# Kernel tuning notes

Hardware: AMD Instinct MI355X
Metric: run time of the kernel (lower is better)

## Reference

```python
import jax, jax.numpy as jnp
import numpy as np

INV_SQRT2 = np.float32(2.0 ** -0.5)
EPS = 1e-5


def _bn5(x, g, b, m, v):
    # inference-mode BatchNorm3d over channel axis 1 of NCDHW
    r = (1, -1, 1, 1, 1)
    return (x - m.reshape(r)) * (g.reshape(r) * jax.lax.rsqrt(v.reshape(r) + EPS)) + b.reshape(r)


def _conv3d(x, w, b, dil=1, pad=0):
    out = jax.lax.conv_general_dilated(
        x, w, window_strides=(1, 1, 1), padding=[(pad, pad)] * 3,
        rhs_dilation=(dil, dil, dil),
        dimension_numbers=('NCDHW', 'OIDHW', 'NCDHW'))
    return out + b.reshape(1, -1, 1, 1, 1)


def _haar_dwt2(x):
    # pywt dwt2(x, 'haar', axes=(-3,-2)) for even-length axes.
    # axis -3 (D): a = approx, d = detail (pywt sign: (x0 - x1)/sqrt2)
    a = (x[:, :, 0::2] + x[:, :, 1::2]) * INV_SQRT2
    d = (x[:, :, 0::2] - x[:, :, 1::2]) * INV_SQRT2
    # axis -2 (H)
    LL = (a[:, :, :, 0::2] + a[:, :, :, 1::2]) * INV_SQRT2  # 'aa'
    HL = (a[:, :, :, 0::2] - a[:, :, :, 1::2]) * INV_SQRT2  # 'ad'
    LH = (d[:, :, :, 0::2] + d[:, :, :, 1::2]) * INV_SQRT2  # 'da'
    HH = (d[:, :, :, 0::2] - d[:, :, :, 1::2]) * INV_SQRT2  # 'dd'
    return LL, LH, HL, HH


def setup_inputs() -> dict:
    key = jax.random.key(0)
    ks = jax.random.split(key, 12)
    B, C1, D, H, W = 2, 60, 128, 128, 64
    CH, R = 64, 4  # gate channels, CH // reduction_ratio
    f32 = jnp.float32
    inp = {
        'x1': jax.random.normal(ks[0], (B, C1, D // 2, H // 2, W), f32),
        'x2': jax.random.normal(ks[1], (B, 1, D, H, W), f32),
        # BatchNorm3d(4) on dwt features
        'bn_g': jnp.ones(4, f32), 'bn_b': jnp.zeros(4, f32),
        'bn_m': jnp.zeros(4, f32), 'bn_v': jnp.ones(4, f32),
        # BAM channel gate: Linear(64->4), BN1d(4), Linear(4->64)
        'cg_w1': jax.random.normal(ks[2], (R, CH), f32) * 0.05,
        'cg_b1': jnp.zeros(R, f32),
        'cg_bng': jnp.ones(R, f32), 'cg_bnb': jnp.zeros(R, f32),
        'cg_bnm': jnp.zeros(R, f32), 'cg_bnv': jnp.ones(R, f32),
        'cg_w2': jax.random.normal(ks[3], (CH, R), f32) * 0.05,
        'cg_b2': jnp.zeros(CH, f32),
        # BAM spatial gate
        'sg_w0': jax.random.normal(ks[4], (R, CH, 1, 1, 1), f32) * 0.05,
        'sg_b0': jnp.zeros(R, f32),
        'sg_g0': jnp.ones(R, f32), 'sg_be0': jnp.zeros(R, f32),
        'sg_m0': jnp.zeros(R, f32), 'sg_v0': jnp.ones(R, f32),
        'sg_w1': jax.random.normal(ks[5], (R, R, 3, 3, 3), f32) * 0.05,
        'sg_b1': jnp.zeros(R, f32),
        'sg_g1': jnp.ones(R, f32), 'sg_be1': jnp.zeros(R, f32),
        'sg_m1': jnp.zeros(R, f32), 'sg_v1': jnp.ones(R, f32),
        'sg_w2': jax.random.normal(ks[6], (R, R, 3, 3, 3), f32) * 0.05,
        'sg_b2': jnp.zeros(R, f32),
        'sg_g2': jnp.ones(R, f32), 'sg_be2': jnp.zeros(R, f32),
        'sg_m2': jnp.zeros(R, f32), 'sg_v2': jnp.ones(R, f32),
        'sg_w3': jax.random.normal(ks[7], (1, R, 1, 1, 1), f32) * 0.05,
        'sg_b3': jnp.zeros(1, f32),
    }
    return inp


def reference(x1, x2, bn_g, bn_b, bn_m, bn_v,
              cg_w1, cg_b1, cg_bng, cg_bnb, cg_bnm, cg_bnv, cg_w2, cg_b2,
              sg_w0, sg_b0, sg_g0, sg_be0, sg_m0, sg_v0,
              sg_w1, sg_b1, sg_g1, sg_be1, sg_m1, sg_v1,
              sg_w2, sg_b2, sg_g2, sg_be2, sg_m2, sg_v2,
              sg_w3, sg_b3):
    LL, LH, HL, HH = _haar_dwt2(x2)
    dwt = jnp.concatenate([LL, LH, HL, HH], axis=1)          # [B,4,D/2,H/2,W]
    dwt = jax.nn.relu(_bn5(dwt, bn_g, bn_b, bn_m, bn_v))
    feat = jnp.concatenate([dwt, x1], axis=1)                # [B,64,D/2,H/2,W]

    # BAM channel gate
    pooled = feat.mean(axis=(2, 3, 4))                        # [B,64]
    h = pooled @ cg_w1.T + cg_b1
    h = jax.nn.relu((h - cg_bnm) * (cg_bng * jax.lax.rsqrt(cg_bnv + EPS)) + cg_bnb)
    att_c = (h @ cg_w2.T + cg_b2)[:, :, None, None, None]     # [B,64,1,1,1]

    # BAM spatial gate
    s = jax.nn.relu(_bn5(_conv3d(feat, sg_w0, sg_b0), sg_g0, sg_be0, sg_m0, sg_v0))
    s = jax.nn.relu(_bn5(_conv3d(s, sg_w1, sg_b1, dil=4, pad=4), sg_g1, sg_be1, sg_m1, sg_v1))
    s = jax.nn.relu(_bn5(_conv3d(s, sg_w2, sg_b2, dil=4, pad=4), sg_g2, sg_be2, sg_m2, sg_v2))
    att_s = _conv3d(s, sg_w3, sg_b3)                          # [B,1,D/2,H/2,W]

    scale = 1.0 + jax.nn.sigmoid(att_c + att_s)
    return (feat * scale, LL)
```

## Files before the change

kernel.cpp:

```cpp
#include <hip/hip_runtime.h>
#include <math.h>

#define EPSBN 1e-5f

typedef float f32x2 __attribute__((ext_vector_type(2)));
typedef float f32x4 __attribute__((ext_vector_type(4)));

constexpr int B   = 2;
constexpr int C1  = 60;
constexpr int NV  = 64 * 64 * 64;
constexpr int NBa = NV / 1024;
constexpr int NBc = NV / 512;

__global__ __launch_bounds__(256) void kA(
    const float* __restrict__ x1, const float* __restrict__ x2,
    const float* __restrict__ bn_g, const float* __restrict__ bn_b,
    const float* __restrict__ bn_m, const float* __restrict__ bn_v,
    const float* __restrict__ sg_w0, const float* __restrict__ sg_b0,
    const float* __restrict__ sg_g0, const float* __restrict__ sg_be0,
    const float* __restrict__ sg_m0, const float* __restrict__ sg_v0,
    float* __restrict__ s0,
    float* __restrict__ part)
{
    __shared__ float wsumq[64][65];

    const int tid = threadIdx.x;
    const int qid = tid >> 2;

    float dsc[4], dsh[4], c0A[4], c0B[4];
    #pragma unroll
    for (int r = 0; r < 4; ++r) {
        float d = bn_g[r] * rsqrtf(bn_v[r] + EPSBN);
        dsc[r] = d; dsh[r] = bn_b[r] - bn_m[r] * d;
        float sc = sg_g0[r] * rsqrtf(sg_v0[r] + EPSBN);
        c0A[r] = sc; c0B[r] = (sg_b0[r] - sg_m0[r]) * sc + sg_be0[r];
    }

    const int b = blockIdx.y;
    const int v = blockIdx.x * 1024 + tid * 4;
    const int x = v & 63, y = (v >> 6) & 63, z = v >> 12;

    const float* px2 = x2 + (size_t)b * (128 * 128 * 64);
    const size_t i00 = ((size_t)(2 * z) * 128 + 2 * y) * 64 + x;
    const float4 p00 = *(const float4*)(px2 + i00);
    const float4 p01 = *(const float4*)(px2 + i00 + 64);
    const float4 p10 = *(const float4*)(px2 + i00 + 8192);
    const float4 p11 = *(const float4*)(px2 + i00 + 8256);
    const float* q00 = (const float*)&p00; const float* q01 = (const float*)&p01;
    const float* q10 = (const float*)&p10; const float* q11 = (const float*)&p11;

    float tv[4][4];
    #pragma unroll
    for (int vi = 0; vi < 4; ++vi) {
        float a = q00[vi], bb = q01[vi], c = q10[vi], d = q11[vi];
        float LL = 0.5f * (a + bb + c + d);
        float LH = 0.5f * (a + bb - c - d);
        float HL = 0.5f * (a - bb + c - d);
        float HH = 0.5f * (a - bb - c + d);
        tv[vi][0] = fmaxf(LL * dsc[0] + dsh[0], 0.f);
        tv[vi][1] = fmaxf(LH * dsc[1] + dsh[1], 0.f);
        tv[vi][2] = fmaxf(HL * dsc[2] + dsh[2], 0.f);
        tv[vi][3] = fmaxf(HH * dsc[3] + dsh[3], 0.f);
    }

    float acc[4][4] = {};
    #pragma unroll
    for (int c = 0; c < 4; ++c) {
        #pragma unroll
        for (int vi = 0; vi < 4; ++vi) {
            float t = tv[vi][c];
            #pragma unroll
            for (int r = 0; r < 4; ++r) acc[vi][r] += sg_w0[r * 64 + c] * t;
        }
        float rs = tv[0][c] + tv[1][c] + tv[2][c] + tv[3][c];
        rs += __shfl_xor(rs, 1);
        rs += __shfl_xor(rs, 2);
        if ((tid & 3) == 0) wsumq[c][qid] = rs;
    }

    const float* px1 = x1 + (size_t)b * C1 * NV + v;
    #pragma unroll 4
    for (int c = 0; c < C1; ++c) {
        const float4 f = *(const float4*)(px1 + (size_t)c * NV);
        const float* fv = (const float*)&f;
        #pragma unroll
        for (int r = 0; r < 4; ++r) {
            const float w = sg_w0[r * 64 + 4 + c];
            #pragma unroll
            for (int vi = 0; vi < 4; ++vi) acc[vi][r] += w * fv[vi];
        }
        float rs = f.x + f.y + f.z + f.w;
        rs += __shfl_xor(rs, 1);
        rs += __shfl_xor(rs, 2);
        if ((tid & 3) == 0) wsumq[4 + c][qid] = rs;
    }

    float4* ps0 = (float4*)s0 + (size_t)b * NV + v;
    #pragma unroll
    for (int vi = 0; vi < 4; ++vi)
        ps0[vi] = make_float4(fmaxf(acc[vi][0] * c0A[0] + c0B[0], 0.f),
                              fmaxf(acc[vi][1] * c0A[1] + c0B[1], 0.f),
                              fmaxf(acc[vi][2] * c0A[2] + c0B[2], 0.f),
                              fmaxf(acc[vi][3] * c0A[3] + c0B[3], 0.f));

    __syncthreads();
    if (tid < 64) {
        const float* rowp = &wsumq[tid][0];
        float p = 0.f;
        #pragma unroll
        for (int i = 0; i < 64; ++i) p += rowp[i];
        part[((size_t)b * 64 + tid) * NBa + blockIdx.x] = p;
    }
}

__global__ __launch_bounds__(256) void kConv1(
    const float* __restrict__ sin_,
    const float* __restrict__ w, const float* __restrict__ bias,
    const float* __restrict__ g, const float* __restrict__ be,
    const float* __restrict__ m, const float* __restrict__ vv,
    const float* __restrict__ part,
    const float* __restrict__ cg_w1, const float* __restrict__ cg_b1,
    const float* __restrict__ cg_bng, const float* __restrict__ cg_bnb,
    const float* __restrict__ cg_bnm, const float* __restrict__ cg_bnv,
    const float* __restrict__ cg_w2, const float* __restrict__ cg_b2,
    float* __restrict__ ec,
    float* __restrict__ outp)
{
    const int tid = threadIdx.x;
    const int b = blockIdx.y;

    if (blockIdx.x == NBc) {
        __shared__ float pooled[64];
        __shared__ float h[4];
        const int c = tid >> 2, q = tid & 3;
        const float4* pp = (const float4*)(part + ((size_t)b * 64 + c) * NBa + q * 64);
        float sm = 0.f;
        #pragma unroll
        for (int i = 0; i < 16; ++i) { float4 f = pp[i]; sm += f.x + f.y + f.z + f.w; }
        sm += __shfl_xor(sm, 1);
        sm += __shfl_xor(sm, 2);
        if (q == 0) pooled[c] = sm * (1.0f / NV);
        __syncthreads();
        if (tid < 4) {
            float a = cg_b1[tid];
            for (int cc = 0; cc < 64; ++cc) a += pooled[cc] * cg_w1[tid * 64 + cc];
            float sc = cg_bng[tid] * rsqrtf(cg_bnv[tid] + EPSBN);
            h[tid] = fmaxf((a - cg_bnm[tid]) * sc + cg_bnb[tid], 0.f);
        }
        __syncthreads();
        if (tid < 64) {
            float a = cg_b2[tid];
            #pragma unroll
            for (int r = 0; r < 4; ++r) a += h[r] * cg_w2[tid * 4 + r];
            ec[b * 64 + tid] = __expf(-a);
        }
        return;
    }

    __shared__ float4 wl4[108];
    if (tid < 108) {
        const int t = tid >> 2, r = tid & 3;
        wl4[tid] = make_float4(w[r * 108 +      t], w[r * 108 +  27 + t],
                               w[r * 108 + 54 + t], w[r * 108 +  81 + t]);
    }
    float cAr[4], cBr[4];
    #pragma unroll
    for (int r = 0; r < 4; ++r) {
        float sc = g[r] * rsqrtf(vv[r] + EPSBN);
        cAr[r] = sc;
        cBr[r] = (bias[r] - m[r]) * sc + be[r];
    }
    __syncthreads();

    const int v = blockIdx.x * 512 + tid * 2;
    const int x = v & 63, y = (v >> 6) & 63, z = v >> 12;
    const float4* pin = (const float4*)sin_ + (size_t)b * NV;

    float acc[2][4] = {};
    #pragma unroll
    for (int kz = -1; kz <= 1; ++kz) {
        const int zz = z + 4 * kz;
        if ((unsigned)zz >= 64u) continue;
        #pragma unroll
        for (int ky = -1; ky <= 1; ++ky) {
            const int yy = y + 4 * ky;
            if ((unsigned)yy >= 64u) continue;
            #pragma unroll
            for (int kx = -1; kx <= 1; ++kx) {
                const int xx = x + 4 * kx;
                if ((unsigned)xx >= 64u) continue;
                const int t = (kz + 1) * 9 + (ky + 1) * 3 + (kx + 1);
                const int vt = zz * 4096 + yy * 64 + xx;
                const float4 w0 = wl4[t * 4 + 0];
                const float4 w1 = wl4[t * 4 + 1];
                const float4 w2 = wl4[t * 4 + 2];
                const float4 w3 = wl4[t * 4 + 3];
                #pragma unroll
                for (int vi = 0; vi < 2; ++vi) {
                    const float4 tap = pin[vt + vi];
                    acc[vi][0] += w0.x * tap.x + w0.y * tap.y + w0.z * tap.z + w0.w * tap.w;
                    acc[vi][1] += w1.x * tap.x + w1.y * tap.y + w1.z * tap.z + w1.w * tap.w;
                    acc[vi][2] += w2.x * tap.x + w2.y * tap.y + w2.z * tap.z + w2.w * tap.w;
                    acc[vi][3] += w3.x * tap.x + w3.y * tap.y + w3.z * tap.z + w3.w * tap.w;
                }
            }
        }
    }

    float4* po = (float4*)outp + (size_t)b * NV + v;
    #pragma unroll
    for (int vi = 0; vi < 2; ++vi)
        po[vi] = make_float4(fmaxf(acc[vi][0] * cAr[0] + cBr[0], 0.f),
                             fmaxf(acc[vi][1] * cAr[1] + cBr[1], 0.f),
                             fmaxf(acc[vi][2] * cAr[2] + cBr[2], 0.f),
                             fmaxf(acc[vi][3] * cAr[3] + cBr[3], 0.f));
}

__global__ __launch_bounds__(256) void kMulF(
    const float* __restrict__ x1,
    const float* __restrict__ x2,
    const float* __restrict__ bn_g, const float* __restrict__ bn_b,
    const float* __restrict__ bn_m, const float* __restrict__ bn_v,
    const float* __restrict__ s1,
    const float* __restrict__ w, const float* __restrict__ bias,
    const float* __restrict__ g, const float* __restrict__ be,
    const float* __restrict__ m, const float* __restrict__ vv,
    const float* __restrict__ w3, const float* __restrict__ b3,
    const float* __restrict__ ec,
    float* __restrict__ out0,
    float* __restrict__ outLL)
{
    const int tid = threadIdx.x;
    const int b = blockIdx.x >> 9;
    const int vb = (blockIdx.x & 511) * 512;

    __shared__ float4 wl4[108];
    __shared__ float ecs[64];
    __shared__ float esb[512];
    __shared__ float dwtb[512][4];
    if (tid < 108) {
        const int t = tid >> 2, r = tid & 3;
        wl4[tid] = make_float4(w[r * 108 +      t], w[r * 108 +  27 + t],
                               w[r * 108 + 54 + t], w[r * 108 +  81 + t]);
    }
    if (tid < 64) ecs[tid] = ec[b * 64 + tid];
    float cAr[4], cBr[4], w3l[4], dsc[4], dsh[4];
    #pragma unroll
    for (int r = 0; r < 4; ++r) {
        float sc = g[r] * rsqrtf(vv[r] + EPSBN);
        cAr[r] = sc;
        cBr[r] = (bias[r] - m[r]) * sc + be[r];
        w3l[r] = w3[r];
        float d = bn_g[r] * rsqrtf(bn_v[r] + EPSBN);
        dsc[r] = d; dsh[r] = bn_b[r] - bn_m[r] * d;
    }
    const float b3l = b3[0];
    __syncthreads();

    {
        const int v = vb + tid * 2;
        const int x = v & 63, y = (v >> 6) & 63, z = v >> 12;

        const float* px2 = x2 + (size_t)b * (128 * 128 * 64);
        const size_t i00 = ((size_t)(2 * z) * 128 + 2 * y) * 64 + x;
        const float2 p00 = *(const float2*)(px2 + i00);
        const float2 p01 = *(const float2*)(px2 + i00 + 64);
        const float2 p10 = *(const float2*)(px2 + i00 + 8192);
        const float2 p11 = *(const float2*)(px2 + i00 + 8256);
        const float* q00 = (const float*)&p00; const float* q01 = (const float*)&p01;
        const float* q10 = (const float*)&p10; const float* q11 = (const float*)&p11;
        float llv[2];
        #pragma unroll
        for (int vi = 0; vi < 2; ++vi) {
            float a = q00[vi], bb = q01[vi], c = q10[vi], d = q11[vi];
            float LL = 0.5f * (a + bb + c + d);
            float LH = 0.5f * (a + bb - c - d);
            float HL = 0.5f * (a - bb + c - d);
            float HH = 0.5f * (a - bb - c + d);
            llv[vi] = LL;
            float4 tv = make_float4(fmaxf(LL * dsc[0] + dsh[0], 0.f),
                                    fmaxf(LH * dsc[1] + dsh[1], 0.f),
                                    fmaxf(HL * dsc[2] + dsh[2], 0.f),
                                    fmaxf(HH * dsc[3] + dsh[3], 0.f));
            *(float4*)&dwtb[tid * 2 + vi][0] = tv;
        }
        {
            f32x2 ll2 = { llv[0], llv[1] };
            __builtin_nontemporal_store(ll2, (f32x2*)(outLL + (size_t)b * NV + v));
        }

        const float4* pin = (const float4*)s1 + (size_t)b * NV;
        float acc[2][4] = {};
        #pragma unroll
        for (int kz = -1; kz <= 1; ++kz) {
            const int zz = z + 4 * kz;
            if ((unsigned)zz >= 64u) continue;
            #pragma unroll
            for (int ky = -1; ky <= 1; ++ky) {
                const int yy = y + 4 * ky;
                if ((unsigned)yy >= 64u) continue;
                #pragma unroll
                for (int kx = -1; kx <= 1; ++kx) {
                    const int xx = x + 4 * kx;
                    if ((unsigned)xx >= 64u) continue;
                    const int t = (kz + 1) * 9 + (ky + 1) * 3 + (kx + 1);
                    const int vt = zz * 4096 + yy * 64 + xx;
                    const float4 w0 = wl4[t * 4 + 0];
                    const float4 w1 = wl4[t * 4 + 1];
                    const float4 w2 = wl4[t * 4 + 2];
                    const float4 w3q = wl4[t * 4 + 3];
                    #pragma unroll
                    for (int vi = 0; vi < 2; ++vi) {
                        const float4 tap = pin[vt + vi];
                        acc[vi][0] += w0.x * tap.x + w0.y * tap.y + w0.z * tap.z + w0.w * tap.w;
                        acc[vi][1] += w1.x * tap.x + w1.y * tap.y + w1.z * tap.z + w1.w * tap.w;
                        acc[vi][2] += w2.x * tap.x + w2.y * tap.y + w2.z * tap.z + w2.w * tap.w;
                        acc[vi][3] += w3q.x * tap.x + w3q.y * tap.y + w3q.z * tap.z + w3q.w * tap.w;
                    }
                }
            }
        }
        #pragma unroll
        for (int vi = 0; vi < 2; ++vi) {
            float r0 = fmaxf(acc[vi][0] * cAr[0] + cBr[0], 0.f);
            float r1 = fmaxf(acc[vi][1] * cAr[1] + cBr[1], 0.f);
            float r2 = fmaxf(acc[vi][2] * cAr[2] + cBr[2], 0.f);
            float r3 = fmaxf(acc[vi][3] * cAr[3] + cBr[3], 0.f);
            esb[tid * 2 + vi] =
                __expf(-(b3l + w3l[0] * r0 + w3l[1] * r1 + w3l[2] * r2 + w3l[3] * r3));
        }
    }
    __syncthreads();

    const int q = tid & 127;
    const int v = vb + q * 4;
    const int ch0 = (tid >> 7) * 32;
    const float es0 = esb[q * 4 + 0], es1 = esb[q * 4 + 1];
    const float es2 = esb[q * 4 + 2], es3 = esb[q * 4 + 3];

    float* po = out0 + ((size_t)b * 64 + ch0) * NV + v;

    if (ch0 == 0) {
        float4 dq0 = *(const float4*)&dwtb[q * 4 + 0][0];
        float4 dq1 = *(const float4*)&dwtb[q * 4 + 1][0];
        float4 dq2 = *(const float4*)&dwtb[q * 4 + 2][0];
        float4 dq3 = *(const float4*)&dwtb[q * 4 + 3][0];
        const float dv0[4] = { dq0.x, dq0.y, dq0.z, dq0.w };
        const float dv1[4] = { dq1.x, dq1.y, dq1.z, dq1.w };
        const float dv2[4] = { dq2.x, dq2.y, dq2.z, dq2.w };
        const float dv3[4] = { dq3.x, dq3.y, dq3.z, dq3.w };
        #pragma unroll
        for (int cc = 0; cc < 4; ++cc) {
            const float e = ecs[cc];
            f32x4 o;
            o.x = dv0[cc] * (1.f + __builtin_amdgcn_rcpf(1.f + e * es0));
            o.y = dv1[cc] * (1.f + __builtin_amdgcn_rcpf(1.f + e * es1));
            o.z = dv2[cc] * (1.f + __builtin_amdgcn_rcpf(1.f + e * es2));
            o.w = dv3[cc] * (1.f + __builtin_amdgcn_rcpf(1.f + e * es3));
            __builtin_nontemporal_store(o, (f32x4*)(po + (size_t)cc * NV));
        }
        const float* px = x1 + (size_t)b * C1 * NV + v;
        #pragma unroll 7
        for (int cc = 4; cc < 32; ++cc) {
            const float4 in4 = *(const float4*)(px + (size_t)(cc - 4) * NV);
            const float e = ecs[cc];
            f32x4 o;
            o.x = in4.x * (1.f + __builtin_amdgcn_rcpf(1.f + e * es0));
            o.y = in4.y * (1.f + __builtin_amdgcn_rcpf(1.f + e * es1));
            o.z = in4.z * (1.f + __builtin_amdgcn_rcpf(1.f + e * es2));
            o.w = in4.w * (1.f + __builtin_amdgcn_rcpf(1.f + e * es3));
            __builtin_nontemporal_store(o, (f32x4*)(po + (size_t)cc * NV));
        }
    } else {
        const float* px = x1 + ((size_t)b * C1 + 28) * NV + v;
        #pragma unroll 8
        for (int cc = 0; cc < 32; ++cc) {
            const float4 in4 = *(const float4*)(px + (size_t)cc * NV);
            const float e = ecs[32 + cc];
            f32x4 o;
            o.x = in4.x * (1.f + __builtin_amdgcn_rcpf(1.f + e * es0));
            o.y = in4.y * (1.f + __builtin_amdgcn_rcpf(1.f + e * es1));
            o.z = in4.z * (1.f + __builtin_amdgcn_rcpf(1.f + e * es2));
            o.w = in4.w * (1.f + __builtin_amdgcn_rcpf(1.f + e * es3));
            __builtin_nontemporal_store(o, (f32x4*)(po + (size_t)cc * NV));
        }
    }
}

extern "C" void kernel_launch(void* const* d_in, const int* in_sizes, int n_in,
                              void* d_out, int out_size, void* d_ws, size_t ws_size,
                              hipStream_t stream)
{
    const float* x1 = (const float*)d_in[0];
    const float* x2 = (const float*)d_in[1];
    const float* bn_g = (const float*)d_in[2];
    const float* bn_b = (const float*)d_in[3];
    const float* bn_m = (const float*)d_in[4];
    const float* bn_v = (const float*)d_in[5];
    const float* cg_w1 = (const float*)d_in[6];
    const float* cg_b1 = (const float*)d_in[7];
    const float* cg_bng = (const float*)d_in[8];
    const float* cg_bnb = (const float*)d_in[9];
    const float* cg_bnm = (const float*)d_in[10];
    const float* cg_bnv = (const float*)d_in[11];
    const float* cg_w2 = (const float*)d_in[12];
    const float* cg_b2 = (const float*)d_in[13];
    const float* sg_w0 = (const float*)d_in[14];
    const float* sg_b0 = (const float*)d_in[15];
    const float* sg_g0 = (const float*)d_in[16];
    const float* sg_be0 = (const float*)d_in[17];
    const float* sg_m0 = (const float*)d_in[18];
    const float* sg_v0 = (const float*)d_in[19];
    const float* sg_w1 = (const float*)d_in[20];
    const float* sg_b1 = (const float*)d_in[21];
    const float* sg_g1 = (const float*)d_in[22];
    const float* sg_be1 = (const float*)d_in[23];
    const float* sg_m1 = (const float*)d_in[24];
    const float* sg_v1 = (const float*)d_in[25];
    const float* sg_w2 = (const float*)d_in[26];
    const float* sg_b2 = (const float*)d_in[27];
    const float* sg_g2 = (const float*)d_in[28];
    const float* sg_be2 = (const float*)d_in[29];
    const float* sg_m2 = (const float*)d_in[30];
    const float* sg_v2 = (const float*)d_in[31];
    const float* sg_w3 = (const float*)d_in[32];
    const float* sg_b3 = (const float*)d_in[33];

    float* ws = (float*)d_ws;
    float* s0   = ws;
    float* s1   = ws + 2097152;
    float* part = ws + 4194304;
    float* ec   = ws + 4227072;

    float* out0  = (float*)d_out;
    float* outLL = out0 + (size_t)B * 64 * NV;

    dim3 blk(256);
    kA<<<dim3(NBa, B), blk, 0, stream>>>(x1, x2, bn_g, bn_b, bn_m, bn_v,
                                         sg_w0, sg_b0, sg_g0, sg_be0, sg_m0, sg_v0,
                                         s0, part);
    kConv1<<<dim3(NBc + 1, B), blk, 0, stream>>>(s0, sg_w1, sg_b1, sg_g1, sg_be1, sg_m1, sg_v1,
                                                 part, cg_w1, cg_b1, cg_bng, cg_bnb, cg_bnm, cg_bnv,
                                                 cg_w2, cg_b2, ec, s1);
    kMulF<<<dim3(1024), blk, 0, stream>>>(x1, x2, bn_g, bn_b, bn_m, bn_v,
                                          s1, sg_w2, sg_b2, sg_g2, sg_be2, sg_m2, sg_v2,
                                          sg_w3, sg_b3, ec, out0, outLL);
}
```

Measured before the change: 99.12 us.

## Fuse three stage kernels into one cooperative kernel with grid syncs

Replaces the three-kernel launch sequence (pointwise conv+DWT, dilated conv1 with channel MLP, dilated conv2 with final multiply) with a single cooperative kernel of 1024 blocks that uses grid.sync between stages. Each block keeps the same 512-voxel slice across all stages, and the channel-gate MLP is computed by slice-0 blocks during the conv1 stage. The aim is to remove inter-kernel launch gaps and tail effects. The cost is that grid syncs require every block to be resident at once and limit occupancy to 4 blocks per CU. If the cooperative launch fails, it falls back to the old three kernels.

```diff
diff --git a/kernel.cpp b/kernel.cpp
--- a/kernel.cpp
+++ b/kernel.cpp
@@ -1,5 +1,8 @@
 #include <hip/hip_runtime.h>
+#include <hip/hip_cooperative_groups.h>
 #include <math.h>
+
+namespace cg = cooperative_groups;
 
 #define EPSBN 1e-5f
 
@@ -9,8 +12,337 @@
 constexpr int B   = 2;
 constexpr int C1  = 60;
 constexpr int NV  = 64 * 64 * 64;
+constexpr int NSL = 512;
+constexpr int GRID = B * NSL;
 constexpr int NBa = NV / 1024;
 constexpr int NBc = NV / 512;
+
+struct Params {
+    const float *x1, *x2;
+    const float *bn_g, *bn_b, *bn_m, *bn_v;
+    const float *cg_w1, *cg_b1, *cg_bng, *cg_bnb, *cg_bnm, *cg_bnv, *cg_w2, *cg_b2;
+    const float *sg_w0, *sg_b0, *sg_g0, *sg_be0, *sg_m0, *sg_v0;
+    const float *sg_w1, *sg_b1, *sg_g1, *sg_be1, *sg_m1, *sg_v1;
+    const float *sg_w2, *sg_b2, *sg_g2, *sg_be2, *sg_m2, *sg_v2;
+    const float *sg_w3, *sg_b3;
+    float *s0, *s1, *part, *ec, *out0, *outLL;
+};
+
+__global__ __launch_bounds__(256, 4) void kFused(Params p)
+{
+    cg::grid_group grid = cg::this_grid();
+
+    const int tid   = threadIdx.x;
+    const int slice = blockIdx.x;
+    const int b     = slice >> 9;
+    const int sIdx  = slice & 511;
+    const int vb    = sIdx * 512;
+
+    __shared__ float  sA[64 * 65];
+    __shared__ float4 wl4a[108], wl4b[108];
+    __shared__ float  ecs[64];
+    __shared__ float  pooled[64], hmlp[4];
+
+    if (tid < 108) {
+        const int t = tid >> 2, r = tid & 3;
+        wl4a[tid] = make_float4(p.sg_w1[r*108+t],    p.sg_w1[r*108+27+t],
+                                p.sg_w1[r*108+54+t], p.sg_w1[r*108+81+t]);
+        wl4b[tid] = make_float4(p.sg_w2[r*108+t],    p.sg_w2[r*108+27+t],
+                                p.sg_w2[r*108+54+t], p.sg_w2[r*108+81+t]);
+    }
+
+    const int v2 = vb + tid * 2;
+    const int x = v2 & 63, y = (v2 >> 6) & 63, z = v2 >> 12;
+
+    {
+        float dsc[4], dsh[4], c0A[4], c0B[4];
+        #pragma unroll
+        for (int r = 0; r < 4; ++r) {
+            float d = p.bn_g[r] * rsqrtf(p.bn_v[r] + EPSBN);
+            dsc[r] = d; dsh[r] = p.bn_b[r] - p.bn_m[r] * d;
+            float sc = p.sg_g0[r] * rsqrtf(p.sg_v0[r] + EPSBN);
+            c0A[r] = sc; c0B[r] = (p.sg_b0[r] - p.sg_m0[r]) * sc + p.sg_be0[r];
+        }
+
+        const float* px2 = p.x2 + (size_t)b * (128*128*64);
+        const size_t i00 = ((size_t)(2*z)*128 + 2*y) * 64 + x;
+        const float2 p00 = *(const float2*)(px2 + i00);
+        const float2 p01 = *(const float2*)(px2 + i00 + 64);
+        const float2 p10 = *(const float2*)(px2 + i00 + 8192);
+        const float2 p11 = *(const float2*)(px2 + i00 + 8256);
+        const float* q00=(const float*)&p00; const float* q01=(const float*)&p01;
+        const float* q10=(const float*)&p10; const float* q11=(const float*)&p11;
+
+        float tv[2][4];
+        #pragma unroll
+        for (int vi = 0; vi < 2; ++vi) {
+            float a=q00[vi], bb=q01[vi], c=q10[vi], d=q11[vi];
+            float LL=0.5f*(a+bb+c+d), LH=0.5f*(a+bb-c-d);
+            float HL=0.5f*(a-bb+c-d), HH=0.5f*(a-bb-c+d);
+            tv[vi][0]=fmaxf(LL*dsc[0]+dsh[0],0.f);
+            tv[vi][1]=fmaxf(LH*dsc[1]+dsh[1],0.f);
+            tv[vi][2]=fmaxf(HL*dsc[2]+dsh[2],0.f);
+            tv[vi][3]=fmaxf(HH*dsc[3]+dsh[3],0.f);
+        }
+
+        float acc[2][4] = {};
+        #pragma unroll
+        for (int c = 0; c < 4; ++c) {
+            #pragma unroll
+            for (int vi = 0; vi < 2; ++vi) {
+                float t = tv[vi][c];
+                #pragma unroll
+                for (int r = 0; r < 4; ++r) acc[vi][r] += p.sg_w0[r*64+c] * t;
+            }
+            float rs = tv[0][c] + tv[1][c];
+            rs += __shfl_xor(rs, 1);
+            rs += __shfl_xor(rs, 2);
+            if ((tid & 3) == 0) sA[c*65 + (tid >> 2)] = rs;
+        }
+
+        const float* px1 = p.x1 + (size_t)b * C1 * NV + v2;
+        #pragma unroll 4
+        for (int c = 0; c < C1; ++c) {
+            const float2 f = *(const float2*)(px1 + (size_t)c * NV);
+            #pragma unroll
+            for (int r = 0; r < 4; ++r) {
+                const float w = p.sg_w0[r*64+4+c];
+                acc[0][r] += w * f.x;
+                acc[1][r] += w * f.y;
+            }
+            float rs = f.x + f.y;
+            rs += __shfl_xor(rs, 1);
+            rs += __shfl_xor(rs, 2);
+            if ((tid & 3) == 0) sA[(4+c)*65 + (tid >> 2)] = rs;
+        }
+
+        float4* ps0 = (float4*)p.s0 + (size_t)b * NV + v2;
+        #pragma unroll
+        for (int vi = 0; vi < 2; ++vi)
+            ps0[vi] = make_float4(fmaxf(acc[vi][0]*c0A[0]+c0B[0],0.f),
+                                  fmaxf(acc[vi][1]*c0A[1]+c0B[1],0.f),
+                                  fmaxf(acc[vi][2]*c0A[2]+c0B[2],0.f),
+                                  fmaxf(acc[vi][3]*c0A[3]+c0B[3],0.f));
+        __syncthreads();
+        if (tid < 64) {
+            const float* rowp = &sA[tid*65];
+            float s = 0.f;
+            #pragma unroll
+            for (int i = 0; i < 64; ++i) s += rowp[i];
+            p.part[((size_t)b*64 + tid) * NSL + sIdx] = s;
+        }
+    }
+
+    grid.sync();
+
+    {
+        float cAr[4], cBr[4];
+        #pragma unroll
+        for (int r = 0; r < 4; ++r) {
+            float sc = p.sg_g1[r] * rsqrtf(p.sg_v1[r] + EPSBN);
+            cAr[r] = sc;
+            cBr[r] = (p.sg_b1[r] - p.sg_m1[r]) * sc + p.sg_be1[r];
+        }
+        const float4* pin = (const float4*)p.s0 + (size_t)b * NV;
+        float acc[2][4] = {};
+        #pragma unroll
+        for (int kz = -1; kz <= 1; ++kz) {
+            const int zz = z + 4*kz;
+            if ((unsigned)zz >= 64u) continue;
+            #pragma unroll
+            for (int ky = -1; ky <= 1; ++ky) {
+                const int yy = y + 4*ky;
+                if ((unsigned)yy >= 64u) continue;
+                #pragma unroll
+                for (int kx = -1; kx <= 1; ++kx) {
+                    const int xx = x + 4*kx;
+                    if ((unsigned)xx >= 64u) continue;
+                    const int t = (kz+1)*9 + (ky+1)*3 + (kx+1);
+                    const int vt = zz*4096 + yy*64 + xx;
+                    const float4 w0 = wl4a[t*4+0], w1 = wl4a[t*4+1];
+                    const float4 w2 = wl4a[t*4+2], w3 = wl4a[t*4+3];
+                    #pragma unroll
+                    for (int vi = 0; vi < 2; ++vi) {
+                        const float4 tap = pin[vt + vi];
+                        acc[vi][0] += w0.x*tap.x + w0.y*tap.y + w0.z*tap.z + w0.w*tap.w;
+                        acc[vi][1] += w1.x*tap.x + w1.y*tap.y + w1.z*tap.z + w1.w*tap.w;
+                        acc[vi][2] += w2.x*tap.x + w2.y*tap.y + w2.z*tap.z + w2.w*tap.w;
+                        acc[vi][3] += w3.x*tap.x + w3.y*tap.y + w3.z*tap.z + w3.w*tap.w;
+                    }
+                }
+            }
+        }
+        float4* po = (float4*)p.s1 + (size_t)b * NV + v2;
+        #pragma unroll
+        for (int vi = 0; vi < 2; ++vi)
+            po[vi] = make_float4(fmaxf(acc[vi][0]*cAr[0]+cBr[0],0.f),
+                                 fmaxf(acc[vi][1]*cAr[1]+cBr[1],0.f),
+                                 fmaxf(acc[vi][2]*cAr[2]+cBr[2],0.f),
+                                 fmaxf(acc[vi][3]*cAr[3]+cBr[3],0.f));
+
+        if (sIdx == 0) {
+            const int c = tid >> 2, q = tid & 3;
+            const float4* pp = (const float4*)(p.part + ((size_t)b*64 + c) * NSL + q*128);
+            float sm = 0.f;
+            #pragma unroll
+            for (int i = 0; i < 32; ++i) { float4 f = pp[i]; sm += f.x+f.y+f.z+f.w; }
+            sm += __shfl_xor(sm, 1);
+            sm += __shfl_xor(sm, 2);
+            if (q == 0) pooled[c] = sm * (1.0f / NV);
+            __syncthreads();
+            if (tid < 4) {
+                float a = p.cg_b1[tid];
+                for (int cc = 0; cc < 64; ++cc) a += pooled[cc] * p.cg_w1[tid*64+cc];
+                float sc = p.cg_bng[tid] * rsqrtf(p.cg_bnv[tid] + EPSBN);
+                hmlp[tid] = fmaxf((a - p.cg_bnm[tid]) * sc + p.cg_bnb[tid], 0.f);
+            }
+            __syncthreads();
+            if (tid < 64) {
+                float a = p.cg_b2[tid];
+                #pragma unroll
+                for (int r = 0; r < 4; ++r) a += hmlp[r] * p.cg_w2[tid*4+r];
+                p.ec[b*64 + tid] = __expf(-a);
+            }
+        }
+    }
+
+    grid.sync();
+
+    float* esb = sA;
+    float (*dwtb)[4] = (float(*)[4])(sA + 512);
+    if (tid < 64) ecs[tid] = p.ec[b*64 + tid];
+    {
+        float cAr[4], cBr[4], w3l[4], dsc[4], dsh[4];
+        #pragma unroll
+        for (int r = 0; r < 4; ++r) {
+            float sc = p.sg_g2[r] * rsqrtf(p.sg_v2[r] + EPSBN);
+            cAr[r] = sc;
+            cBr[r] = (p.sg_b2[r] - p.sg_m2[r]) * sc + p.sg_be2[r];
+            w3l[r] = p.sg_w3[r];
+            float d = p.bn_g[r] * rsqrtf(p.bn_v[r] + EPSBN);
+            dsc[r] = d; dsh[r] = p.bn_b[r] - p.bn_m[r] * d;
+        }
+        const float b3l = p.sg_b3[0];
+
+        const float* px2 = p.x2 + (size_t)b * (128*128*64);
+        const size_t i00 = ((size_t)(2*z)*128 + 2*y) * 64 + x;
+        const float2 p00 = *(const float2*)(px2 + i00);
+        const float2 p01 = *(const float2*)(px2 + i00 + 64);
+        const float2 p10 = *(const float2*)(px2 + i00 + 8192);
+        const float2 p11 = *(const float2*)(px2 + i00 + 8256);
+        const float* q00=(const float*)&p00; const float* q01=(const float*)&p01;
+        const float* q10=(const float*)&p10; const float* q11=(const float*)&p11;
+        float llv[2];
+        #pragma unroll
+        for (int vi = 0; vi < 2; ++vi) {
+            float a=q00[vi], bb=q01[vi], c=q10[vi], d=q11[vi];
+            float LL=0.5f*(a+bb+c+d), LH=0.5f*(a+bb-c-d);
+            float HL=0.5f*(a-bb+c-d), HH=0.5f*(a-bb-c+d);
+            llv[vi] = LL;
+            float4 tv = make_float4(fmaxf(LL*dsc[0]+dsh[0],0.f), fmaxf(LH*dsc[1]+dsh[1],0.f),
+                                    fmaxf(HL*dsc[2]+dsh[2],0.f), fmaxf(HH*dsc[3]+dsh[3],0.f));
+            *(float4*)&dwtb[tid*2+vi][0] = tv;
+        }
+        {
+            f32x2 ll2 = { llv[0], llv[1] };
+            __builtin_nontemporal_store(ll2, (f32x2*)(p.outLL + (size_t)b*NV + v2));
+        }
+
+        const float4* pin = (const float4*)p.s1 + (size_t)b * NV;
+        float acc[2][4] = {};
+        #pragma unroll
+        for (int kz = -1; kz <= 1; ++kz) {
+            const int zz = z + 4*kz;
+            if ((unsigned)zz >= 64u) continue;
+            #pragma unroll
+            for (int ky = -1; ky <= 1; ++ky) {
+                const int yy = y + 4*ky;
+                if ((unsigned)yy >= 64u) continue;
+                #pragma unroll
+                for (int kx = -1; kx <= 1; ++kx) {
+                    const int xx = x + 4*kx;
+                    if ((unsigned)xx >= 64u) continue;
+                    const int t = (kz+1)*9 + (ky+1)*3 + (kx+1);
+                    const int vt = zz*4096 + yy*64 + xx;
+                    const float4 w0 = wl4b[t*4+0], w1 = wl4b[t*4+1];
+                    const float4 w2 = wl4b[t*4+2], w3q = wl4b[t*4+3];
+                    #pragma unroll
+                    for (int vi = 0; vi < 2; ++vi) {
+                        const float4 tap = pin[vt + vi];
+                        acc[vi][0] += w0.x*tap.x + w0.y*tap.y + w0.z*tap.z + w0.w*tap.w;
+                        acc[vi][1] += w1.x*tap.x + w1.y*tap.y + w1.z*tap.z + w1.w*tap.w;
+                        acc[vi][2] += w2.x*tap.x + w2.y*tap.y + w2.z*tap.z + w2.w*tap.w;
+                        acc[vi][3] += w3q.x*tap.x + w3q.y*tap.y + w3q.z*tap.z + w3q.w*tap.w;
+                    }
+                }
+            }
+        }
+        #pragma unroll
+        for (int vi = 0; vi < 2; ++vi) {
+            float r0 = fmaxf(acc[vi][0]*cAr[0]+cBr[0],0.f);
+            float r1 = fmaxf(acc[vi][1]*cAr[1]+cBr[1],0.f);
+            float r2 = fmaxf(acc[vi][2]*cAr[2]+cBr[2],0.f);
+            float r3 = fmaxf(acc[vi][3]*cAr[3]+cBr[3],0.f);
+            esb[tid*2+vi] = __expf(-(b3l + w3l[0]*r0 + w3l[1]*r1 + w3l[2]*r2 + w3l[3]*r3));
+        }
+    }
+    __syncthreads();
+
+    {
+        const int q = tid & 127;
+        const int v4 = vb + q * 4;
+        const int ch0 = (tid >> 7) * 32;
+        const float es0 = esb[q*4+0], es1 = esb[q*4+1];
+        const float es2 = esb[q*4+2], es3 = esb[q*4+3];
+        float* po = p.out0 + ((size_t)b*64 + ch0) * NV + v4;
+
+        if (ch0 == 0) {
+            float4 dq0 = *(const float4*)&dwtb[q*4+0][0];
+            float4 dq1 = *(const float4*)&dwtb[q*4+1][0];
+            float4 dq2 = *(const float4*)&dwtb[q*4+2][0];
+            float4 dq3 = *(const float4*)&dwtb[q*4+3][0];
+            const float dv0[4] = { dq0.x, dq0.y, dq0.z, dq0.w };
+            const float dv1[4] = { dq1.x, dq1.y, dq1.z, dq1.w };
+            const float dv2[4] = { dq2.x, dq2.y, dq2.z, dq2.w };
+            const float dv3[4] = { dq3.x, dq3.y, dq3.z, dq3.w };
+            #pragma unroll
+            for (int cc = 0; cc < 4; ++cc) {
+                const float e = ecs[cc];
+                f32x4 o;
+                o.x = dv0[cc] * (1.f + __builtin_amdgcn_rcpf(1.f + e*es0));
+                o.y = dv1[cc] * (1.f + __builtin_amdgcn_rcpf(1.f + e*es1));
+                o.z = dv2[cc] * (1.f + __builtin_amdgcn_rcpf(1.f + e*es2));
+                o.w = dv3[cc] * (1.f + __builtin_amdgcn_rcpf(1.f + e*es3));
+                __builtin_nontemporal_store(o, (f32x4*)(po + (size_t)cc * NV));
+            }
+            const float* px = p.x1 + (size_t)b * C1 * NV + v4;
+            #pragma unroll 7
+            for (int cc = 4; cc < 32; ++cc) {
+                const float4 in4 = *(const float4*)(px + (size_t)(cc-4) * NV);
+                const float e = ecs[cc];
+                f32x4 o;
+                o.x = in4.x * (1.f + __builtin_amdgcn_rcpf(1.f + e*es0));
+                o.y = in4.y * (1.f + __builtin_amdgcn_rcpf(1.f + e*es1));
+                o.z = in4.z * (1.f + __builtin_amdgcn_rcpf(1.f + e*es2));
+                o.w = in4.w * (1.f + __builtin_amdgcn_rcpf(1.f + e*es3));
+                __builtin_nontemporal_store(o, (f32x4*)(po + (size_t)cc * NV));
+            }
+        } else {
+            const float* px = p.x1 + ((size_t)b * C1 + 28) * NV + v4;
+            #pragma unroll 8
+            for (int cc = 0; cc < 32; ++cc) {
+                const float4 in4 = *(const float4*)(px + (size_t)cc * NV);
+                const float e = ecs[32 + cc];
+                f32x4 o;
+                o.x = in4.x * (1.f + __builtin_amdgcn_rcpf(1.f + e*es0));
+                o.y = in4.y * (1.f + __builtin_amdgcn_rcpf(1.f + e*es1));
+                o.z = in4.z * (1.f + __builtin_amdgcn_rcpf(1.f + e*es2));
+                o.w = in4.w * (1.f + __builtin_amdgcn_rcpf(1.f + e*es3));
+                __builtin_nontemporal_store(o, (f32x4*)(po + (size_t)cc * NV));
+            }
+        }
+    }
+}
 
 __global__ __launch_bounds__(256) void kA(
     const float* __restrict__ x1, const float* __restrict__ x2,
@@ -391,58 +723,69 @@
                               void* d_out, int out_size, void* d_ws, size_t ws_size,
                               hipStream_t stream)
 {
-    const float* x1 = (const float*)d_in[0];
-    const float* x2 = (const float*)d_in[1];
-    const float* bn_g = (const float*)d_in[2];
-    const float* bn_b = (const float*)d_in[3];
-    const float* bn_m = (const float*)d_in[4];
-    const float* bn_v = (const float*)d_in[5];
-    const float* cg_w1 = (const float*)d_in[6];
-    const float* cg_b1 = (const float*)d_in[7];
-    const float* cg_bng = (const float*)d_in[8];
-    const float* cg_bnb = (const float*)d_in[9];
-    const float* cg_bnm = (const float*)d_in[10];
-    const float* cg_bnv = (const float*)d_in[11];
-    const float* cg_w2 = (const float*)d_in[12];
-    const float* cg_b2 = (const float*)d_in[13];
-    const float* sg_w0 = (const float*)d_in[14];
-    const float* sg_b0 = (const float*)d_in[15];
-    const float* sg_g0 = (const float*)d_in[16];
-    const float* sg_be0 = (const float*)d_in[17];
-    const float* sg_m0 = (const float*)d_in[18];
-    const float* sg_v0 = (const float*)d_in[19];
-    const float* sg_w1 = (const float*)d_in[20];
-    const float* sg_b1 = (const float*)d_in[21];
-    const float* sg_g1 = (const float*)d_in[22];
-    const float* sg_be1 = (const float*)d_in[23];
-    const float* sg_m1 = (const float*)d_in[24];
-    const float* sg_v1 = (const float*)d_in[25];
-    const float* sg_w2 = (const float*)d_in[26];
-    const float* sg_b2 = (const float*)d_in[27];
-    const float* sg_g2 = (const float*)d_in[28];
-    const float* sg_be2 = (const float*)d_in[29];
-    const float* sg_m2 = (const float*)d_in[30];
-    const float* sg_v2 = (const float*)d_in[31];
-    const float* sg_w3 = (const float*)d_in[32];
-    const float* sg_b3 = (const float*)d_in[33];
-
     float* ws = (float*)d_ws;
-    float* s0   = ws;
-    float* s1   = ws + 2097152;
-    float* part = ws + 4194304;
-    float* ec   = ws + 4227072;
-
     float* out0  = (float*)d_out;
-    float* outLL = out0 + (size_t)B * 64 * NV;
-
-    dim3 blk(256);
-    kA<<<dim3(NBa, B), blk, 0, stream>>>(x1, x2, bn_g, bn_b, bn_m, bn_v,
-                                         sg_w0, sg_b0, sg_g0, sg_be0, sg_m0, sg_v0,
-                                         s0, part);
-    kConv1<<<dim3(NBc + 1, B), blk, 0, stream>>>(s0, sg_w1, sg_b1, sg_g1, sg_be1, sg_m1, sg_v1,
-                                                 part, cg_w1, cg_b1, cg_bng, cg_bnb, cg_bnm, cg_bnv,
-                                                 cg_w2, cg_b2, ec, s1);
-    kMulF<<<dim3(1024), blk, 0, stream>>>(x1, x2, bn_g, bn_b, bn_m, bn_v,
-                                          s1, sg_w2, sg_b2, sg_g2, sg_be2, sg_m2, sg_v2,
-                                          sg_w3, sg_b3, ec, out0, outLL);
+
+    Params p;
+    p.x1 = (const float*)d_in[0];
+    p.x2 = (const float*)d_in[1];
+    p.bn_g = (const float*)d_in[2];
+    p.bn_b = (const float*)d_in[3];
+    p.bn_m = (const float*)d_in[4];
+    p.bn_v = (const float*)d_in[5];
+    p.cg_w1 = (const float*)d_in[6];
+    p.cg_b1 = (const float*)d_in[7];
+    p.cg_bng = (const float*)d_in[8];
+    p.cg_bnb = (const float*)d_in[9];
+    p.cg_bnm = (const float*)d_in[10];
+    p.cg_bnv = (const float*)d_in[11];
+    p.cg_w2 = (const float*)d_in[12];
+    p.cg_b2 = (const float*)d_in[13];
+    p.sg_w0 = (const float*)d_in[14];
+    p.sg_b0 = (const float*)d_in[15];
+    p.sg_g0 = (const float*)d_in[16];
+    p.sg_be0 = (const float*)d_in[17];
+    p.sg_m0 = (const float*)d_in[18];
+    p.sg_v0 = (const float*)d_in[19];
+    p.sg_w1 = (const float*)d_in[20];
+    p.sg_b1 = (const float*)d_in[21];
+    p.sg_g1 = (const float*)d_in[22];
+    p.sg_be1 = (const float*)d_in[23];
+    p.sg_m1 = (const float*)d_in[24];
+    p.sg_v1 = (const float*)d_in[25];
+    p.sg_w2 = (const float*)d_in[26];
+    p.sg_b2 = (const float*)d_in[27];
+    p.sg_g2 = (const float*)d_in[28];
+    p.sg_be2 = (const float*)d_in[29];
+    p.sg_m2 = (const float*)d_in[30];
+    p.sg_v2 = (const float*)d_in[31];
+    p.sg_w3 = (const float*)d_in[32];
+    p.sg_b3 = (const float*)d_in[33];
+
+    p.s0   = ws;
+    p.s1   = ws + 2097152;
+    p.part = ws + 4194304;
+    p.ec   = ws + 4259840;
+    p.out0  = out0;
+    p.outLL = out0 + (size_t)B * 64 * NV;
+
+    void* args[] = { &p };
+    hipError_t err = hipLaunchCooperativeKernel((const void*)kFused, dim3(GRID), dim3(256),
+                                                args, 0, stream);
+    if (err != hipSuccess) {
+        (void)hipGetLastError();
+        dim3 blk(256);
+        kA<<<dim3(NBa, B), blk, 0, stream>>>(p.x1, p.x2, p.bn_g, p.bn_b, p.bn_m, p.bn_v,
+                                             p.sg_w0, p.sg_b0, p.sg_g0, p.sg_be0, p.sg_m0, p.sg_v0,
+                                             p.s0, p.part);
+        kConv1<<<dim3(NBc + 1, B), blk, 0, stream>>>(p.s0, p.sg_w1, p.sg_b1, p.sg_g1, p.sg_be1,
+                                                     p.sg_m1, p.sg_v1,
+                                                     p.part, p.cg_w1, p.cg_b1, p.cg_bng, p.cg_bnb,
+                                                     p.cg_bnm, p.cg_bnv, p.cg_w2, p.cg_b2,
+                                                     p.ec, p.s1);
+        kMulF<<<dim3(1024), blk, 0, stream>>>(p.x1, p.x2, p.bn_g, p.bn_b, p.bn_m, p.bn_v,
+                                              p.s1, p.sg_w2, p.sg_b2, p.sg_g2, p.sg_be2,
+                                              p.sg_m2, p.sg_v2,
+                                              p.sg_w3, p.sg_b3, p.ec, p.out0, p.outLL);
+    }
 }
```

Result: slower. 376.3 us (+279.6%).
